# Kernel tuning notes

Hardware: AMD Instinct MI355X
Metric: run time of the kernel (lower is better)

Reference implementation:

```python
import jax, jax.numpy as jnp
import numpy as np

# ---- dims ----
N_NODES = 33      # nodes per graph (33-bus grid)
SEQ     = 24      # time steps per sample
BATCH   = 64      # samples
G       = BATCH * SEQ          # total graphs in the batch
EPG     = 64                   # directed edges per graph
E       = G * EPG              # total edges
N       = G * N_NODES          # total nodes
IN_CH   = 2
HID     = 64
HEADS   = 8
HC      = HID * HEADS          # 512
EDGE_DIM = 3
LSTM1_H = 128
LSTM2_H = 64
N_CLASSES = 4
NEG_SLOPE = 0.2


def setup_inputs() -> dict:
    key = jax.random.key(0)
    ks = jax.random.split(key, 32)
    rng = np.random.default_rng(0)

    # block-structured edge_index: every edge stays inside its own graph
    off = np.repeat(np.arange(G, dtype=np.int64) * N_NODES, EPG)
    src = rng.integers(0, N_NODES, E) + off
    dst = rng.integers(0, N_NODES, E) + off
    edge_index = jnp.asarray(np.stack([src, dst]), dtype=jnp.int32)

    def glorot(k, shape):
        fan = shape[0] + shape[-1]
        s = jnp.sqrt(6.0 / fan).astype(jnp.float32)
        return jax.random.uniform(k, shape, jnp.float32, -s, s)

    inp = dict(
        x=jax.random.normal(ks[0], (N, IN_CH), jnp.float32),
        edge_index=edge_index,
        edge_attr=jax.random.uniform(ks[1], (E, EDGE_DIM), jnp.float32),
        # GATv2 layer 1 (concat=True)
        g1_Wl=glorot(ks[2], (IN_CH, HC)),
        g1_Wr=glorot(ks[3], (IN_CH, HC)),
        g1_We=glorot(ks[4], (EDGE_DIM, HC)),
        g1_att=glorot(ks[5], (HEADS, HID)),
        g1_b=jnp.zeros((HC,), jnp.float32),
        # GATv2 layer 2 (concat=False -> head mean)
        g2_Wl=glorot(ks[6], (HC, HC)),
        g2_Wr=glorot(ks[7], (HC, HC)),
        g2_We=glorot(ks[8], (EDGE_DIM, HC)),
        g2_att=glorot(ks[9], (HEADS, HID)),
        g2_b=jnp.zeros((HID,), jnp.float32),
        # LSTM1: input 33*64=2112 -> 128, gates ordered (i,f,g,o)
        l1_Wih=0.05 * jax.random.normal(ks[10], (4 * LSTM1_H, N_NODES * HID), jnp.float32),
        l1_Whh=0.05 * jax.random.normal(ks[11], (4 * LSTM1_H, LSTM1_H), jnp.float32),
        l1_bih=jnp.zeros((4 * LSTM1_H,), jnp.float32),
        l1_bhh=jnp.zeros((4 * LSTM1_H,), jnp.float32),
        # LSTM2: 128 -> 64
        l2_Wih=0.05 * jax.random.normal(ks[12], (4 * LSTM2_H, LSTM1_H), jnp.float32),
        l2_Whh=0.05 * jax.random.normal(ks[13], (4 * LSTM2_H, LSTM2_H), jnp.float32),
        l2_bih=jnp.zeros((4 * LSTM2_H,), jnp.float32),
        l2_bhh=jnp.zeros((4 * LSTM2_H,), jnp.float32),
        # FC 64 -> n_classes
        fc_W=0.05 * jax.random.normal(ks[14], (N_CLASSES, LSTM2_H), jnp.float32),
        fc_b=jnp.zeros((N_CLASSES,), jnp.float32),
    )
    return inp


def _gatv2(x, edge_attr, src, dst, Wl, Wr, We, att, b, concat):
    """PyG GATv2Conv with edge_dim, add_self_loops semantics omitted is NOT used:
    we follow the message math: m = leaky_relu(xl[src]+xr[dst]+We@e),
    alpha = segment_softmax(<m,att>, dst), out = scatter_add(alpha * xl[src])."""
    n = x.shape[0]
    xl = (x @ Wl).reshape(n, HEADS, HID)      # [N,H,C]
    xr = (x @ Wr).reshape(n, HEADS, HID)
    em = (edge_attr @ We).reshape(-1, HEADS, HID)  # [E,H,C]
    m = jax.nn.leaky_relu(xl[src] + xr[dst] + em, NEG_SLOPE)
    logits = jnp.einsum('ehc,hc->eh', m, att)          # [E,H]
    mx = jax.ops.segment_max(logits, dst, num_segments=n)   # [N,H]
    ex = jnp.exp(logits - mx[dst])
    den = jax.ops.segment_sum(ex, dst, num_segments=n)
    alpha = ex / (den[dst] + 1e-16)                    # [E,H]
    out = jax.ops.segment_sum(xl[src] * alpha[:, :, None], dst, num_segments=n)  # [N,H,C]
    out = out.reshape(n, HC) if concat else out.mean(axis=1)
    return out + b


def _lstm(x, Wih, Whh, bih, bhh, hsz):
    B = x.shape[0]
    h0 = jnp.zeros((B, hsz), x.dtype)
    c0 = jnp.zeros((B, hsz), x.dtype)

    def step(carry, xt):
        h, c = carry
        gates = xt @ Wih.T + h @ Whh.T + bih + bhh
        i, f, g, o = jnp.split(gates, 4, axis=-1)
        i = jax.nn.sigmoid(i); f = jax.nn.sigmoid(f)
        g = jnp.tanh(g);       o = jax.nn.sigmoid(o)
        c = f * c + i * g
        h = o * jnp.tanh(c)
        return (h, c), h

    _, ys = jax.lax.scan(step, (h0, c0), x.transpose(1, 0, 2))  # [T,B,H]
    return ys.transpose(1, 0, 2)


def reference(x, edge_index, edge_attr,
              g1_Wl, g1_Wr, g1_We, g1_att, g1_b,
              g2_Wl, g2_Wr, g2_We, g2_att, g2_b,
              l1_Wih, l1_Whh, l1_bih, l1_bhh,
              l2_Wih, l2_Whh, l2_bih, l2_bhh,
              fc_W, fc_b):
    src, dst = edge_index[0], edge_index[1]
    h = jax.nn.elu(_gatv2(x, edge_attr, src, dst, g1_Wl, g1_Wr, g1_We, g1_att, g1_b, True))
    h = jax.nn.elu(_gatv2(h, edge_attr, src, dst, g2_Wl, g2_Wr, g2_We, g2_att, g2_b, False))
    seq = h.reshape(BATCH, SEQ, N_NODES * HID)          # [B,T,2112]
    seq = _lstm(seq, l1_Wih, l1_Whh, l1_bih, l1_bhh, LSTM1_H)
    seq = _lstm(seq, l2_Wih, l2_Whh, l2_bih, l2_bhh, LSTM2_H)
    last = seq[:, -1, :]                                 # [B,64]
    return last @ fc_W.T + fc_b                          # [B,n_classes]
```

## Files before the change

kernel.cpp:

```cpp
#include <hip/hip_runtime.h>
#include <math.h>

#define N_NODES 33
#define SEQ 24
#define BATCH 64
#define G_GRAPHS (BATCH * SEQ)
#define EPG 64
#define E_EDGES (G_GRAPHS * EPG)
#define N_TOTAL (G_GRAPHS * N_NODES)
#define HID 64
#define HEADS 8
#define HC (HID * HEADS)
#define LSTM1_H 128
#define LSTM2_H 64
#define NEG_SLOPE 0.2f
#define CONV_BLOCKS (128 + 264)

__device__ __forceinline__ float sigmoidf_(float x) { return 1.f / (1.f + expf(-x)); }
__device__ __forceinline__ float eluf_(float x) { return x > 0.f ? x : expm1f(x); }
__device__ __forceinline__ float lreluf_(float x) { return x > 0.f ? x : NEG_SLOPE * x; }

typedef __attribute__((ext_vector_type(4))) float f32x4;
typedef _Float16 half_t;
typedef __attribute__((ext_vector_type(8))) _Float16 halfx8;

__device__ __forceinline__ void gl2lds16(const void* g, void* l) {
  __builtin_amdgcn_global_load_lds(
      (__attribute__((address_space(1))) const unsigned int*)g,
      (__attribute__((address_space(3))) unsigned int*)l, 16, 0, 0);
}

__global__ __launch_bounds__(512) void gat1_kernel(
    const float* __restrict__ x, const int* __restrict__ src, const int* __restrict__ dst,
    const float* __restrict__ ea, const float* __restrict__ Wl, const float* __restrict__ Wr,
    const float* __restrict__ We, const float* __restrict__ att, const float* __restrict__ bias,
    half_t* __restrict__ h1, int g0, int gat_blocks,
    const float* __restrict__ g2Wl, const float* __restrict__ g2Wr,
    half_t* __restrict__ B2, const float* __restrict__ W1, half_t* __restrict__ W1f) {
  const int tid = threadIdx.x;

  __shared__ alignas(16) float Wl_s[2 * 512];
  __shared__ alignas(16) float Wr_s[2 * 512];
  __shared__ alignas(16) float We_s[3 * 512];
  __shared__ alignas(16) float att_s[512];
  __shared__ float xs0_s[N_NODES + 1], xs1_s[N_NODES + 1];
  __shared__ float easX[EPG], easY[EPG], easZ[EPG];
  __shared__ float logit_s[HEADS * 65];
  __shared__ int sloc[EPG], dloc[EPG], deg[N_NODES], start[N_NODES], fill[N_NODES], elist[EPG];
  __shared__ float tr[64 * 65];

  if ((int)blockIdx.x >= gat_blocks) {
    int cb = blockIdx.x - gat_blocks;
    if (cb < 128) {
      int kt = cb & 7, nt = cb >> 3;
      int k0 = kt * 64, n0 = nt * 64;
      int r = tid >> 6, c = tid & 63;
      #pragma unroll
      for (int rr = 0; rr < 8; ++rr) {
        int kl = rr * 8 + r;
        int n = n0 + c;
        float v = (n < 512) ? g2Wl[(size_t)(k0 + kl) * 512 + n]
                            : g2Wr[(size_t)(k0 + kl) * 512 + n - 512];
        tr[kl * 65 + c] = v;
      }
      __syncthreads();
      #pragma unroll
      for (int rr = 0; rr < 8; ++rr) {
        int nl = rr * 8 + r;
        B2[(size_t)(n0 + nl) * 512 + k0 + c] = (half_t)tr[c * 65 + nl];
      }
    } else {
      int base = (cb - 128) * 4096 + tid;
      #pragma unroll
      for (int i = 0; i < 8; ++i) {
        int idx = base + i * 512;
        if (idx < 512 * 2112) W1f[idx] = (half_t)W1[idx];
      }
    }
    return;
  }

  const int g = g0 + blockIdx.x;
  const int nb = g * N_NODES, eb = g * EPG;
  const int lb = blockIdx.x * N_NODES;

  for (int i = tid; i < 1024; i += 512) { Wl_s[i] = Wl[i]; Wr_s[i] = Wr[i]; }
  for (int i = tid; i < 1536; i += 512) We_s[i] = We[i];
  if (tid < 512) att_s[tid] = att[tid];
  if (tid < 2 * N_NODES) {
    float v = x[nb * 2 + tid];
    if (tid & 1) xs1_s[tid >> 1] = v; else xs0_s[tid >> 1] = v;
  }
  if (tid < EPG) {
    easX[tid] = ea[(eb + tid) * 3 + 0];
    easY[tid] = ea[(eb + tid) * 3 + 1];
    easZ[tid] = ea[(eb + tid) * 3 + 2];
    sloc[tid] = src[eb + tid] - nb;
    dloc[tid] = dst[eb + tid] - nb;
  }
  if (tid < N_NODES) { deg[tid] = 0; fill[tid] = 0; }
  __syncthreads();
  if (tid < EPG) atomicAdd(&deg[dloc[tid]], 1);
  __syncthreads();
  if (tid == 0) { int a = 0; for (int n = 0; n < N_NODES; ++n) { start[n] = a; a += deg[n]; } }
  __syncthreads();
  if (tid < EPG) { int d = dloc[tid]; int p = atomicAdd(&fill[d], 1); elist[start[d] + p] = tid; }

  {
    int h = tid >> 6, e = tid & 63;
    int s = sloc[e], d = dloc[e];
    float xs0 = xs0_s[s], xs1 = xs1_s[s], xd0 = xs0_s[d], xd1 = xs1_s[d];
    float e0 = easX[e], e1 = easY[e], e2 = easZ[e];
    float acc = 0.f;
    int base = h * 64;
    #pragma unroll
    for (int c4 = 0; c4 < 16; ++c4) {
      int j = base + c4 * 4;
      f32x4 wl0 = *(const f32x4*)(Wl_s + j);
      f32x4 wl1 = *(const f32x4*)(Wl_s + 512 + j);
      f32x4 wr0 = *(const f32x4*)(Wr_s + j);
      f32x4 wr1 = *(const f32x4*)(Wr_s + 512 + j);
      f32x4 we0 = *(const f32x4*)(We_s + j);
      f32x4 we1 = *(const f32x4*)(We_s + 512 + j);
      f32x4 we2 = *(const f32x4*)(We_s + 1024 + j);
      f32x4 at  = *(const f32x4*)(att_s + j);
      #pragma unroll
      for (int q = 0; q < 4; ++q) {
        float v = xs0 * wl0[q] + xs1 * wl1[q]
                + xd0 * wr0[q] + xd1 * wr1[q]
                + e0 * we0[q] + e1 * we1[q] + e2 * we2[q];
        acc += lreluf_(v) * at[q];
      }
    }
    logit_s[h * 65 + e] = acc;
  }
  __syncthreads();

  {
    int h = tid >> 6, n = tid & 63;
    if (n < N_NODES) {
      int s0 = start[n], dn = deg[n];
      float mx = -1e30f;
      for (int i = 0; i < dn; ++i) mx = fmaxf(mx, logit_s[h * 65 + elist[s0 + i]]);
      float den = 0.f;
      for (int i = 0; i < dn; ++i) den += expf(logit_s[h * 65 + elist[s0 + i]] - mx);
      float inv = 1.f / (den + 1e-16f);
      for (int i = 0; i < dn; ++i) {
        int e = elist[s0 + i];
        logit_s[h * 65 + e] = expf(logit_s[h * 65 + e] - mx) * inv;
      }
    }
  }
  __syncthreads();

  for (int t = tid; t < N_NODES * 64; t += 512) {
    int n = t >> 6, jb = t & 63;
    int j0 = jb * 8, h = jb >> 3;
    f32x4 wa0 = *(const f32x4*)(Wl_s + j0);
    f32x4 wa1 = *(const f32x4*)(Wl_s + j0 + 4);
    f32x4 wb0 = *(const f32x4*)(Wl_s + 512 + j0);
    f32x4 wb1 = *(const f32x4*)(Wl_s + 512 + j0 + 4);
    float acc[8] = {};
    int s0 = start[n], dn = deg[n];
    for (int i = 0; i < dn; ++i) {
      int e = elist[s0 + i]; int s = sloc[e];
      float a = logit_s[h * 65 + e];
      float ax0 = a * xs0_s[s], ax1 = a * xs1_s[s];
      #pragma unroll
      for (int q = 0; q < 4; ++q) {
        acc[q]     += ax0 * wa0[q] + ax1 * wb0[q];
        acc[4 + q] += ax0 * wa1[q] + ax1 * wb1[q];
      }
    }
    f32x4 b0 = *(const f32x4*)(bias + j0);
    f32x4 b1 = *(const f32x4*)(bias + j0 + 4);
    halfx8 vh;
    #pragma unroll
    for (int cc = 0; cc < 8; ++cc) {
      float bb = (cc < 4) ? b0[cc] : b1[cc - 4];
      vh[cc] = (half_t)eluf_(acc[cc] + bb);
    }
    *(halfx8*)(h1 + (size_t)(lb + n) * HC + j0) = vh;
  }
}

template <int WM, int WN, int NP, int K, int SA, int SB, typename TC>
__global__ __launch_bounds__(256) void gemm_f16(
    const half_t* __restrict__ A, const half_t* __restrict__ B,
    TC* __restrict__ C, const float* __restrict__ bias1, const float* __restrict__ bias2,
    int M, int N) {
  constexpr int BM = 32 * WM, BN = 32 * WN;
  constexpr bool BOUNCE = (sizeof(TC) == 2) && (BM == 128) && (BN == 128);
  constexpr int STAGE_HALFS = (BM + BN) * 32 * NP;
  constexpr int CT_HALFS = BOUNCE ? 128 * 132 : 0;
  constexpr int LDS_HALFS = STAGE_HALFS > CT_HALFS ? STAGE_HALFS : CT_HALFS;
  __shared__ half_t lds[LDS_HALFS];
  half_t* A_s = lds;
  half_t* B_s = A_s + NP * BM * 32;

  const int R = M / BM, NT = N / BN;
  int b = blockIdx.x;
  int xcd = b & 7, q = b >> 3;
  int ct = q % NT, rg = q / NT;
  int r = rg * 8 + xcd;
  if (r >= R) return;

  const int tid = threadIdx.x;
  const int wave = tid >> 6, lane = tid & 63;
  const int wm = wave >> 1, wn = wave & 1;
  const int bm = r * BM, bn = ct * BN;

  const int rA = lane >> 2;
  const int swz = (rA & 3) ^ ((rA >> 2) & 3);
  const int cA = ((lane & 3) ^ swz) * 8;

  f32x4 acc[WM][WN];
  #pragma unroll
  for (int tm = 0; tm < WM; ++tm)
    #pragma unroll
    for (int tn = 0; tn < WN; ++tn) acc[tm][tn] = {0.f, 0.f, 0.f, 0.f};

  for (int k0 = 0; k0 < K; k0 += 32 * NP) {
    #pragma unroll
    for (int p = 0; p < NP; ++p) {
      int kk = k0 + p * 32;
      #pragma unroll
      for (int i = 0; i < BM / 64; ++i) {
        int row = i * 64 + wave * 16;
        gl2lds16(A + (size_t)(bm + row + rA) * SA + kk + cA,
                 A_s + p * BM * 32 + row * 32);
      }
      #pragma unroll
      for (int i = 0; i < BN / 64; ++i) {
        int row = i * 64 + wave * 16;
        gl2lds16(B + (size_t)(bn + row + rA) * SB + kk + cA,
                 B_s + p * BN * 32 + row * 32);
      }
    }
    __syncthreads();

    const int fr = lane & 15;
    const int fs = (fr & 3) ^ ((fr >> 2) & 3);
    const int fk = ((lane >> 4) ^ fs) * 8;
    #pragma unroll
    for (int p = 0; p < NP; ++p) {
      const int pA = p * BM * 32, pB = p * BN * 32;
      halfx8 af[WM], bf[WN];
      #pragma unroll
      for (int tm = 0; tm < WM; ++tm) {
        int rr = (wm * WM + tm) * 16 + fr;
        af[tm] = *(const halfx8*)(A_s + pA + rr * 32 + fk);
      }
      #pragma unroll
      for (int tn = 0; tn < WN; ++tn) {
        int rr = (wn * WN + tn) * 16 + fr;
        bf[tn] = *(const halfx8*)(B_s + pB + rr * 32 + fk);
      }
      #pragma unroll
      for (int tm = 0; tm < WM; ++tm)
        #pragma unroll
        for (int tn = 0; tn < WN; ++tn)
          acc[tm][tn] = __builtin_amdgcn_mfma_f32_16x16x32_f16(af[tm], bf[tn], acc[tm][tn], 0, 0, 0);
    }
    __syncthreads();
  }

  const int col0 = lane & 15, rq = (lane >> 4) * 4;
  if constexpr (BOUNCE) {
    half_t* Cs = lds;
    #pragma unroll
    for (int tm = 0; tm < WM; ++tm)
      #pragma unroll
      for (int tn = 0; tn < WN; ++tn) {
        int cl = (wn * WN + tn) * 16 + col0;
        #pragma unroll
        for (int rr = 0; rr < 4; ++rr) {
          int rl = (wm * WM + tm) * 16 + rq + rr;
          Cs[rl * 132 + cl] = (half_t)acc[tm][tn][rr];
        }
      }
    __syncthreads();
    #pragma unroll
    for (int pass = 0; pass < 8; ++pass) {
      int row = pass * 16 + (tid >> 4);
      int col = (tid & 15) * 8;
      halfx8 v = *(const halfx8*)(Cs + row * 132 + col);
      *(halfx8*)((half_t*)C + (size_t)(bm + row) * N + bn + col) = v;
    }
  } else {
    #pragma unroll
    for (int tm = 0; tm < WM; ++tm)
      #pragma unroll
      for (int tn = 0; tn < WN; ++tn) {
        int col = bn + (wn * WN + tn) * 16 + col0;
        float badd = 0.f;
        if (bias1) badd += bias1[col];
        if (bias2) badd += bias2[col];
        #pragma unroll
        for (int rr = 0; rr < 4; ++rr) {
          int row = bm + (wm * WM + tm) * 16 + rq + rr;
          C[(size_t)row * N + col] = (TC)(acc[tm][tn][rr] + badd);
        }
      }
  }
}

__global__ __launch_bounds__(256) void gemm_f16_splitk(
    const half_t* __restrict__ A, const half_t* __restrict__ B,
    float* __restrict__ Cp, const float* __restrict__ bias1, const float* __restrict__ bias2,
    int M, int N) {
  constexpr int SA = 2112;
  __shared__ half_t lds[(64 + 64) * 64];
  half_t* A_s = lds;
  half_t* B_s = A_s + 2 * 64 * 32;

  const int part = blockIdx.y;
  const int koff = part ? 576 + (part - 1) * 512 : 0;
  const int kend = part ? 512 : 576;
  const half_t* Ap = A + koff;
  const half_t* Bp = B + koff;
  float* C = Cp + (size_t)part * M * N;

  const int R = M / 64, NT = N / 64;
  int b = blockIdx.x;
  int xcd = b & 7, q = b >> 3;
  int ct = q % NT, rg = q / NT;
  int r = rg * 8 + xcd;
  if (r >= R) return;

  const int tid = threadIdx.x;
  const int wave = tid >> 6, lane = tid & 63;
  const int wm = wave >> 1, wn = wave & 1;
  const int bm = r * 64, bn = ct * 64;

  const int rA = lane >> 2;
  const int swz = (rA & 3) ^ ((rA >> 2) & 3);
  const int cA = ((lane & 3) ^ swz) * 8;

  f32x4 acc[2][2];
  #pragma unroll
  for (int tm = 0; tm < 2; ++tm)
    #pragma unroll
    for (int tn = 0; tn < 2; ++tn) acc[tm][tn] = {0.f, 0.f, 0.f, 0.f};

  for (int k0 = 0; k0 < kend; k0 += 64) {
    #pragma unroll
    for (int p = 0; p < 2; ++p) {
      int kk = k0 + p * 32;
      int row = wave * 16;
      gl2lds16(Ap + (size_t)(bm + row + rA) * SA + kk + cA,
               A_s + p * 64 * 32 + row * 32);
      gl2lds16(Bp + (size_t)(bn + row + rA) * SA + kk + cA,
               B_s + p * 64 * 32 + row * 32);
    }
    __syncthreads();
    const int fr = lane & 15;
    const int fs = (fr & 3) ^ ((fr >> 2) & 3);
    const int fk = ((lane >> 4) ^ fs) * 8;
    #pragma unroll
    for (int p = 0; p < 2; ++p) {
      const int pA = p * 64 * 32, pB = p * 64 * 32;
      halfx8 af[2], bf[2];
      #pragma unroll
      for (int tm = 0; tm < 2; ++tm) {
        int rr = (wm * 2 + tm) * 16 + fr;
        af[tm] = *(const halfx8*)(A_s + pA + rr * 32 + fk);
      }
      #pragma unroll
      for (int tn = 0; tn < 2; ++tn) {
        int rr = (wn * 2 + tn) * 16 + fr;
        bf[tn] = *(const halfx8*)(B_s + pB + rr * 32 + fk);
      }
      #pragma unroll
      for (int tm = 0; tm < 2; ++tm)
        #pragma unroll
        for (int tn = 0; tn < 2; ++tn)
          acc[tm][tn] = __builtin_amdgcn_mfma_f32_16x16x32_f16(af[tm], bf[tn], acc[tm][tn], 0, 0, 0);
    }
    __syncthreads();
  }

  const int col0 = lane & 15, rq = (lane >> 4) * 4;
  #pragma unroll
  for (int tm = 0; tm < 2; ++tm)
    #pragma unroll
    for (int tn = 0; tn < 2; ++tn) {
      int col = bn + (wn * 2 + tn) * 16 + col0;
      float badd = (part == 0) ? (bias1[col] + bias2[col]) : 0.f;
      #pragma unroll
      for (int rr = 0; rr < 4; ++rr) {
        int row = bm + (wm * 2 + tm) * 16 + rq + rr;
        C[(size_t)row * N + col] = acc[tm][tn][rr] + badd;
      }
    }
}

__global__ __launch_bounds__(512) void gat2_kernel(
    const half_t* __restrict__ xlr, const int* __restrict__ src, const int* __restrict__ dst,
    const float* __restrict__ ea, const float* __restrict__ We,
    const float* __restrict__ att, const float* __restrict__ bias,
    half_t* __restrict__ h2, int g0) {
  __shared__ alignas(16) float We_s[3 * 512];
  __shared__ alignas(16) float att_s[512];
  __shared__ float b_s[HID];
  __shared__ float easX[EPG], easY[EPG], easZ[EPG];
  __shared__ float logit_s[HEADS * 65];
  __shared__ int sloc[EPG], dloc[EPG], deg[N_NODES], start[N_NODES], fill[N_NODES], elist[EPG];

  const int g = g0 + blockIdx.x, tid = threadIdx.x;
  const int nb = g * N_NODES, eb = g * EPG;
  const int lb = blockIdx.x * N_NODES;
  const int wave = tid >> 6, lane = tid & 63;

  for (int i = tid; i < 1536; i += 512) We_s[i] = We[i];
  if (tid < 512) att_s[tid] = att[tid];
  if (tid < HID) b_s[tid] = bias[tid];
  if (tid < EPG) {
    easX[tid] = ea[(eb + tid) * 3 + 0];
    easY[tid] = ea[(eb + tid) * 3 + 1];
    easZ[tid] = ea[(eb + tid) * 3 + 2];
    sloc[tid] = src[eb + tid] - nb;
    dloc[tid] = dst[eb + tid] - nb;
  }
  if (tid < N_NODES) { deg[tid] = 0; fill[tid] = 0; }
  __syncthreads();
  if (tid < EPG) atomicAdd(&deg[dloc[tid]], 1);
  __syncthreads();
  if (tid == 0) { int a = 0; for (int n = 0; n < N_NODES; ++n) { start[n] = a; a += deg[n]; } }
  __syncthreads();
  if (tid < EPG) { int d = dloc[tid]; int p = atomicAdd(&fill[d], 1); elist[start[d] + p] = tid; }
  __syncthreads();

  const int j0 = lane * 8;
  float w0[8], w1[8], w2[8], at8[8];
  #pragma unroll
  for (int q = 0; q < 8; ++q) {
    w0[q] = We_s[j0 + q];
    w1[q] = We_s[512 + j0 + q];
    w2[q] = We_s[1024 + j0 + q];
    at8[q] = att_s[j0 + q];
  }

  for (int e = wave; e < EPG; e += 8) {
    int s = sloc[e], d = dloc[e];
    halfx8 xlv = *((const halfx8*)(xlr + (size_t)(lb + s) * 1024) + lane);
    halfx8 xrv = *((const halfx8*)(xlr + (size_t)(lb + d) * 1024 + 512) + lane);
    float e0 = easX[e], e1 = easY[e], e2 = easZ[e];
    float acc = 0.f;
    #pragma unroll
    for (int q = 0; q < 8; ++q) {
      float v = (float)xlv[q] + (float)xrv[q] + e0 * w0[q] + e1 * w1[q] + e2 * w2[q];
      acc += lreluf_(v) * at8[q];
    }
    acc += __shfl_xor(acc, 1, 64);
    acc += __shfl_xor(acc, 2, 64);
    acc += __shfl_xor(acc, 4, 64);
    if ((lane & 7) == 0) logit_s[(lane >> 3) * 65 + e] = acc;
  }
  __syncthreads();

  {
    int h = tid >> 6, n = tid & 63;
    if (n < N_NODES) {
      int s0 = start[n], dn = deg[n];
      float mx = -1e30f;
      for (int i = 0; i < dn; ++i) mx = fmaxf(mx, logit_s[h * 65 + elist[s0 + i]]);
      float den = 0.f;
      for (int i = 0; i < dn; ++i) den += expf(logit_s[h * 65 + elist[s0 + i]] - mx);
      float inv = 1.f / (den + 1e-16f);
      for (int i = 0; i < dn; ++i) {
        int e = elist[s0 + i];
        logit_s[h * 65 + e] = expf(logit_s[h * 65 + e] - mx) * inv;
      }
    }
  }
  __syncthreads();

  for (int n = wave; n < N_NODES; n += 8) {
    float acc = 0.f;
    int s0 = start[n], dn = deg[n];
    for (int i = 0; i < dn; ++i) {
      int e = elist[s0 + i], s = sloc[e];
      const half_t* row = xlr + (size_t)(lb + s) * 1024 + lane;
      #pragma unroll
      for (int h = 0; h < 8; ++h)
        acc += logit_s[h * 65 + e] * (float)row[h * 64];
    }
    float v = eluf_(acc * 0.125f + b_s[lane]);
    h2[(size_t)(nb + n) * HID + lane] = (half_t)v;
  }
}

__global__ __launch_bounds__(1024, 4) void lstm_all(
    const float* __restrict__ X0, const float* __restrict__ X1,
    const float* __restrict__ X2p, const float* __restrict__ X3,
    const float* __restrict__ Whh1,
    const float* __restrict__ Wih2, const float* __restrict__ bih2,
    const float* __restrict__ bhh2, const float* __restrict__ Whh2,
    const float* __restrict__ fcW, const float* __restrict__ fcb,
    float* __restrict__ out) {
  __shared__ float hs1[LSTM1_H], cs1[LSTM1_H], p1[512], gs1[512];
  __shared__ float Y1s[SEQ][LSTM1_H];
  __shared__ float hs2[LSTM2_H], cs2[LSTM2_H], p2[4 * 256], gs2[256];
  const int tid = threadIdx.x, b = blockIdx.x;
  const int j = tid & 511, half = tid >> 9;

  float4 w1[16];
  {
    const float4* wp = (const float4*)(Whh1 + (size_t)j * LSTM1_H + half * 64);
    #pragma unroll
    for (int q = 0; q < 16; ++q) w1[q] = wp[q];
  }
  if (tid < LSTM1_H) { hs1[tid] = 0.f; cs1[tid] = 0.f; }
  __syncthreads();
  for (int t = 0; t < SEQ; ++t) {
    const float* hb = hs1 + half * 64;
    float acc = 0.f;
    #pragma unroll
    for (int q = 0; q < 16; ++q) {
      acc += w1[q].x * hb[4 * q] + w1[q].y * hb[4 * q + 1]
           + w1[q].z * hb[4 * q + 2] + w1[q].w * hb[4 * q + 3];
    }
    if (half) p1[j] = acc;
    __syncthreads();
    if (!half) {
      size_t xo = ((size_t)b * SEQ + t) * 512 + j;
      gs1[j] = acc + p1[j] + X0[xo] + X1[xo] + X2p[xo] + X3[xo];
    }
    __syncthreads();
    if (tid < LSTM1_H) {
      float ig = sigmoidf_(gs1[tid]);
      float fg = sigmoidf_(gs1[LSTM1_H + tid]);
      float gg = tanhf(gs1[2 * LSTM1_H + tid]);
      float og = sigmoidf_(gs1[3 * LSTM1_H + tid]);
      float c = fg * cs1[tid] + ig * gg;
      cs1[tid] = c;
      float h = og * tanhf(c);
      hs1[tid] = h;
      Y1s[t][tid] = h;
    }
    __syncthreads();
  }

  const int j2 = tid & 255, qt = tid >> 8;
  float4 w2x[8], w2h[4];
  {
    const float4* wxp = (const float4*)(Wih2 + (size_t)j2 * LSTM1_H + qt * 32);
    #pragma unroll
    for (int q = 0; q < 8; ++q) w2x[q] = wxp[q];
    const float4* whp = (const float4*)(Whh2 + (size_t)j2 * LSTM2_H + qt * 16);
    #pragma unroll
    for (int q = 0; q < 4; ++q) w2h[q] = whp[q];
  }
  if (tid < LSTM2_H) { hs2[tid] = 0.f; cs2[tid] = 0.f; }
  __syncthreads();
  for (int t = 0; t < SEQ; ++t) {
    const float* y = Y1s[t] + qt * 32;
    const float* hb = hs2 + qt * 16;
    float acc = 0.f;
    #pragma unroll
    for (int q = 0; q < 8; ++q) {
      acc += w2x[q].x * y[4 * q] + w2x[q].y * y[4 * q + 1]
           + w2x[q].z * y[4 * q + 2] + w2x[q].w * y[4 * q + 3];
    }
    #pragma unroll
    for (int q = 0; q < 4; ++q) {
      acc += w2h[q].x * hb[4 * q] + w2h[q].y * hb[4 * q + 1]
           + w2h[q].z * hb[4 * q + 2] + w2h[q].w * hb[4 * q + 3];
    }
    p2[qt * 256 + j2] = acc;
    __syncthreads();
    if (qt == 0)
      gs2[j2] = p2[j2] + p2[256 + j2] + p2[512 + j2] + p2[768 + j2]
              + bih2[j2] + bhh2[j2];
    __syncthreads();
    if (tid < LSTM2_H) {
      float ig = sigmoidf_(gs2[tid]);
      float fg = sigmoidf_(gs2[LSTM2_H + tid]);
      float gg = tanhf(gs2[2 * LSTM2_H + tid]);
      float og = sigmoidf_(gs2[3 * LSTM2_H + tid]);
      float c = fg * cs2[tid] + ig * gg;
      cs2[tid] = c;
      hs2[tid] = og * tanhf(c);
    }
    __syncthreads();
  }
  if (tid < 4) {
    float acc = fcb[tid];
    #pragma unroll
    for (int k = 0; k < LSTM2_H; ++k) acc += fcW[tid * LSTM2_H + k] * hs2[k];
    out[b * 4 + tid] = acc;
  }
}

extern "C" void kernel_launch(void* const* d_in, const int* in_sizes, int n_in,
                              void* d_out, int out_size, void* d_ws, size_t ws_size,
                              hipStream_t stream) {
  const float* x       = (const float*)d_in[0];
  const int*   eidx    = (const int*)d_in[1];
  const float* eattr   = (const float*)d_in[2];
  const float* g1_Wl   = (const float*)d_in[3];
  const float* g1_Wr   = (const float*)d_in[4];
  const float* g1_We   = (const float*)d_in[5];
  const float* g1_att  = (const float*)d_in[6];
  const float* g1_b    = (const float*)d_in[7];
  const float* g2_Wl   = (const float*)d_in[8];
  const float* g2_Wr   = (const float*)d_in[9];
  const float* g2_We   = (const float*)d_in[10];
  const float* g2_att  = (const float*)d_in[11];
  const float* g2_b    = (const float*)d_in[12];
  const float* l1_Wih  = (const float*)d_in[13];
  const float* l1_Whh  = (const float*)d_in[14];
  const float* l1_bih  = (const float*)d_in[15];
  const float* l1_bhh  = (const float*)d_in[16];
  const float* l2_Wih  = (const float*)d_in[17];
  const float* l2_Whh  = (const float*)d_in[18];
  const float* l2_bih  = (const float*)d_in[19];
  const float* l2_bhh  = (const float*)d_in[20];
  const float* fc_W    = (const float*)d_in[21];
  const float* fc_b    = (const float*)d_in[22];
  float* out = (float*)d_out;

  const int* src = eidx;
  const int* dst = eidx + E_EDGES;

  const int cand[5] = {1, 2, 3, 4, 6};
  int nchunks = 0;
  half_t *h1 = nullptr, *xlr2c = nullptr, *h2 = nullptr, *B2 = nullptr, *W1f = nullptr;
  float *X1p = nullptr;
  int chunk_g = 0, chunk_n = 0;
  for (int ci = 0; ci < 5; ++ci) {
    int C = cand[ci];
    int CG = G_GRAPHS / C, CN = CG * N_NODES;
    char* p = (char*)d_ws;
    auto alloc = [&](size_t bytes) { char* r = p; p += (bytes + 255) & ~(size_t)255; return r; };
    half_t* t_h1    = (half_t*)alloc((size_t)CN * HC * 2);
    half_t* t_xlr2c = (half_t*)alloc((size_t)CN * 1024 * 2);
    half_t* t_h2    = (half_t*)alloc((size_t)G_GRAPHS * 2112 * 2);
    half_t* t_B2    = (half_t*)alloc((size_t)1024 * 512 * 2);
    half_t* t_W1f   = (half_t*)alloc((size_t)512 * 2112 * 2);
    float*  t_X1p   = (float*)alloc((size_t)4 * G_GRAPHS * 512 * 4);
    if ((size_t)(p - (char*)d_ws) <= ws_size) {
      nchunks = C; chunk_g = CG; chunk_n = CN;
      h1 = t_h1; xlr2c = t_xlr2c; h2 = t_h2; B2 = t_B2; W1f = t_W1f;
      X1p = t_X1p;
      break;
    }
  }
  if (nchunks == 0) return;

  for (int c = 0; c < nchunks; ++c) {
    int g0 = c * chunk_g;
    int extra = (c == 0) ? CONV_BLOCKS : 0;
    gat1_kernel<<<chunk_g + extra, 512, 0, stream>>>(
        x, src, dst, eattr, g1_Wl, g1_Wr, g1_We, g1_att, g1_b, h1, g0, chunk_g,
        g2_Wl, g2_Wr, B2, l1_Wih, W1f);
    int R = chunk_n / 128, NT = 1024 / 128;
    int gblocks = 8 * ((R + 7) / 8) * NT;
    gemm_f16<4, 4, 2, HC, HC, HC, half_t><<<gblocks, 256, 0, stream>>>(
        h1, B2, xlr2c, (const float*)nullptr, (const float*)nullptr,
        chunk_n, 1024);
    gat2_kernel<<<chunk_g, 512, 0, stream>>>(xlr2c, src, dst, eattr, g2_We,
                                             g2_att, g2_b, h2, g0);
  }

  {
    dim3 grid(192, 4);
    gemm_f16_splitk<<<grid, 256, 0, stream>>>(h2, W1f, X1p, l1_bih, l1_bhh,
                                              G_GRAPHS, 512);
  }

  {
    size_t PS = (size_t)G_GRAPHS * 512;
    lstm_all<<<BATCH, 1024, 0, stream>>>(X1p, X1p + PS, X1p + 2 * PS, X1p + 3 * PS,
                                         l1_Whh, l2_Wih, l2_bih, l2_bhh, l2_Whh,
                                         fc_W, fc_b, out);
  }
}
```

Measured before the change: 349.1 us.

## Replace layer-2 projection GEMM with 256x256 tile, 4-stage pipelined kernel

Swaps the templated 128x128 GEMM that computes the layer-2 left/right projections for a dedicated 256x256-tile kernel. It uses 512 threads, a 4-slot LDS ring with 3 tiles of prefetch gated by explicit vmcnt waits, and raised wave priority around the MFMA block. The larger tile halves global re-reads of A and B per output, and the deeper pipeline overlaps loads with compute. The cost is a full 128 KB of LDS and 128 accumulator registers per lane, which limits occupancy. The chunk candidate 4 is dropped so that chunk node counts stay divisible by 256.

New measurement: 359.5 us. 1.03x slower.

```diff
diff --git a/kernel.cpp b/kernel.cpp
--- a/kernel.cpp
+++ b/kernel.cpp
@@ -184,124 +184,106 @@
   }
 }
 
-template <int WM, int WN, int NP, int K, int SA, int SB, typename TC>
-__global__ __launch_bounds__(256) void gemm_f16(
+__global__ __launch_bounds__(512, 2) void gemm256(
     const half_t* __restrict__ A, const half_t* __restrict__ B,
-    TC* __restrict__ C, const float* __restrict__ bias1, const float* __restrict__ bias2,
-    int M, int N) {
-  constexpr int BM = 32 * WM, BN = 32 * WN;
-  constexpr bool BOUNCE = (sizeof(TC) == 2) && (BM == 128) && (BN == 128);
-  constexpr int STAGE_HALFS = (BM + BN) * 32 * NP;
-  constexpr int CT_HALFS = BOUNCE ? 128 * 132 : 0;
-  constexpr int LDS_HALFS = STAGE_HALFS > CT_HALFS ? STAGE_HALFS : CT_HALFS;
-  __shared__ half_t lds[LDS_HALFS];
-  half_t* A_s = lds;
-  half_t* B_s = A_s + NP * BM * 32;
-
-  const int R = M / BM, NT = N / BN;
+    half_t* __restrict__ C, int M) {
+  __shared__ alignas(16) half_t lds[65536];
+
+  const int R = M >> 8;
   int b = blockIdx.x;
   int xcd = b & 7, q = b >> 3;
-  int ct = q % NT, rg = q / NT;
+  int ct = q & 3, rg = q >> 2;
   int r = rg * 8 + xcd;
   if (r >= R) return;
 
   const int tid = threadIdx.x;
   const int wave = tid >> 6, lane = tid & 63;
-  const int wm = wave >> 1, wn = wave & 1;
-  const int bm = r * BM, bn = ct * BN;
+  const int wm = wave >> 2, wn = wave & 3;
+  const int bm = r << 8, bn = ct << 8;
 
   const int rA = lane >> 2;
-  const int swz = (rA & 3) ^ ((rA >> 2) & 3);
-  const int cA = ((lane & 3) ^ swz) * 8;
-
-  f32x4 acc[WM][WN];
+  const int swzS = (rA & 3) ^ ((rA >> 2) & 3);
+  const int cA = ((lane & 3) ^ swzS) * 8;
+
+  const int fr = lane & 15;
+  const int fs = (fr & 3) ^ ((fr >> 2) & 3);
+  const int fk = ((lane >> 4) ^ fs) * 8;
+
+  f32x4 acc[8][4];
   #pragma unroll
-  for (int tm = 0; tm < WM; ++tm)
-    #pragma unroll
-    for (int tn = 0; tn < WN; ++tn) acc[tm][tn] = {0.f, 0.f, 0.f, 0.f};
-
-  for (int k0 = 0; k0 < K; k0 += 32 * NP) {
-    #pragma unroll
-    for (int p = 0; p < NP; ++p) {
-      int kk = k0 + p * 32;
-      #pragma unroll
-      for (int i = 0; i < BM / 64; ++i) {
-        int row = i * 64 + wave * 16;
-        gl2lds16(A + (size_t)(bm + row + rA) * SA + kk + cA,
-                 A_s + p * BM * 32 + row * 32);
-      }
-      #pragma unroll
-      for (int i = 0; i < BN / 64; ++i) {
-        int row = i * 64 + wave * 16;
-        gl2lds16(B + (size_t)(bn + row + rA) * SB + kk + cA,
-                 B_s + p * BN * 32 + row * 32);
-      }
-    }
-    __syncthreads();
-
-    const int fr = lane & 15;
-    const int fs = (fr & 3) ^ ((fr >> 2) & 3);
-    const int fk = ((lane >> 4) ^ fs) * 8;
-    #pragma unroll
-    for (int p = 0; p < NP; ++p) {
-      const int pA = p * BM * 32, pB = p * BN * 32;
-      halfx8 af[WM], bf[WN];
-      #pragma unroll
-      for (int tm = 0; tm < WM; ++tm) {
-        int rr = (wm * WM + tm) * 16 + fr;
-        af[tm] = *(const halfx8*)(A_s + pA + rr * 32 + fk);
-      }
-      #pragma unroll
-      for (int tn = 0; tn < WN; ++tn) {
-        int rr = (wn * WN + tn) * 16 + fr;
-        bf[tn] = *(const halfx8*)(B_s + pB + rr * 32 + fk);
-      }
-      #pragma unroll
-      for (int tm = 0; tm < WM; ++tm)
+  for (int tm = 0; tm < 8; ++tm)
+    #pragma unroll
+    for (int tn = 0; tn < 4; ++tn) acc[tm][tn] = {0.f, 0.f, 0.f, 0.f};
+
+  auto stage = [&](int kt, int slot) {
+    half_t* As = lds + slot * 16384;
+    half_t* Bs = As + 8192;
+    const int koff = kt * 32 + cA;
+    #pragma unroll
+    for (int i = 0; i < 2; ++i) {
+      int row = i * 128 + wave * 16;
+      gl2lds16(A + (size_t)(bm + row + rA) * 512 + koff, As + row * 32);
+      gl2lds16(B + (size_t)(bn + row + rA) * 512 + koff, Bs + row * 32);
+    }
+  };
+
+  stage(0, 0);
+  stage(1, 1);
+  stage(2, 2);
+
+  for (int kt = 0; kt < 16; ++kt) {
+    if (kt < 14)       asm volatile("s_waitcnt vmcnt(8)" ::: "memory");
+    else if (kt == 14) asm volatile("s_waitcnt vmcnt(4)" ::: "memory");
+    else               asm volatile("s_waitcnt vmcnt(0)" ::: "memory");
+    __builtin_amdgcn_s_barrier();
+    asm volatile("" ::: "memory");
+
+    if (kt + 3 < 16) stage(kt + 3, (kt + 3) & 3);
+
+    const half_t* As = lds + (kt & 3) * 16384;
+    const half_t* Bs = As + 8192;
+
+    halfx8 bf[4];
+    #pragma unroll
+    for (int tn = 0; tn < 4; ++tn)
+      bf[tn] = *(const halfx8*)(Bs + (wn * 64 + tn * 16 + fr) * 32 + fk);
+
+    __builtin_amdgcn_s_setprio(1);
+    #pragma unroll
+    for (int tm = 0; tm < 8; ++tm) {
+      halfx8 af = *(const halfx8*)(As + (wm * 128 + tm * 16 + fr) * 32 + fk);
+      #pragma unroll
+      for (int tn = 0; tn < 4; ++tn)
+        acc[tm][tn] = __builtin_amdgcn_mfma_f32_16x16x32_f16(af, bf[tn], acc[tm][tn], 0, 0, 0);
+    }
+    __builtin_amdgcn_s_setprio(0);
+  }
+
+  half_t* Cs = lds;
+  const int rq = (lane >> 4) * 4;
+  const int cl0 = lane & 15;
+  #pragma unroll 1
+  for (int mh = 0; mh < 2; ++mh) {
+    __syncthreads();
+    if (wm == mh) {
+      #pragma unroll
+      for (int tm = 0; tm < 8; ++tm)
         #pragma unroll
-        for (int tn = 0; tn < WN; ++tn)
-          acc[tm][tn] = __builtin_amdgcn_mfma_f32_16x16x32_f16(af[tm], bf[tn], acc[tm][tn], 0, 0, 0);
-    }
-    __syncthreads();
-  }
-
-  const int col0 = lane & 15, rq = (lane >> 4) * 4;
-  if constexpr (BOUNCE) {
-    half_t* Cs = lds;
-    #pragma unroll
-    for (int tm = 0; tm < WM; ++tm)
-      #pragma unroll
-      for (int tn = 0; tn < WN; ++tn) {
-        int cl = (wn * WN + tn) * 16 + col0;
-        #pragma unroll
-        for (int rr = 0; rr < 4; ++rr) {
-          int rl = (wm * WM + tm) * 16 + rq + rr;
-          Cs[rl * 132 + cl] = (half_t)acc[tm][tn][rr];
+        for (int tn = 0; tn < 4; ++tn) {
+          int cl = wn * 64 + tn * 16 + cl0;
+          #pragma unroll
+          for (int rr = 0; rr < 4; ++rr)
+            Cs[(tm * 16 + rq + rr) * 264 + cl] = (half_t)acc[tm][tn][rr];
         }
-      }
-    __syncthreads();
-    #pragma unroll
-    for (int pass = 0; pass < 8; ++pass) {
-      int row = pass * 16 + (tid >> 4);
-      int col = (tid & 15) * 8;
-      halfx8 v = *(const halfx8*)(Cs + row * 132 + col);
-      *(halfx8*)((half_t*)C + (size_t)(bm + row) * N + bn + col) = v;
-    }
-  } else {
-    #pragma unroll
-    for (int tm = 0; tm < WM; ++tm)
-      #pragma unroll
-      for (int tn = 0; tn < WN; ++tn) {
-        int col = bn + (wn * WN + tn) * 16 + col0;
-        float badd = 0.f;
-        if (bias1) badd += bias1[col];
-        if (bias2) badd += bias2[col];
-        #pragma unroll
-        for (int rr = 0; rr < 4; ++rr) {
-          int row = bm + (wm * WM + tm) * 16 + rq + rr;
-          C[(size_t)row * N + col] = (TC)(acc[tm][tn][rr] + badd);
-        }
-      }
+    }
+    __syncthreads();
+    #pragma unroll
+    for (int i = 0; i < 8; ++i) {
+      int rr2 = i * 16 + (tid >> 5);
+      int cc = (tid & 31) * 8;
+      halfx8 v = *(const halfx8*)(Cs + rr2 * 264 + cc);
+      *(halfx8*)(C + (size_t)(bm + mh * 128 + rr2) * 1024 + bn + cc) = v;
+    }
   }
 }
 
@@ -624,12 +606,12 @@
   const int* src = eidx;
   const int* dst = eidx + E_EDGES;
 
-  const int cand[5] = {1, 2, 3, 4, 6};
+  const int cand[4] = {1, 2, 3, 6};
   int nchunks = 0;
   half_t *h1 = nullptr, *xlr2c = nullptr, *h2 = nullptr, *B2 = nullptr, *W1f = nullptr;
   float *X1p = nullptr;
   int chunk_g = 0, chunk_n = 0;
-  for (int ci = 0; ci < 5; ++ci) {
+  for (int ci = 0; ci < 4; ++ci) {
     int C = cand[ci];
     int CG = G_GRAPHS / C, CN = CG * N_NODES;
     char* p = (char*)d_ws;
@@ -655,11 +637,9 @@
     gat1_kernel<<<chunk_g + extra, 512, 0, stream>>>(
         x, src, dst, eattr, g1_Wl, g1_Wr, g1_We, g1_att, g1_b, h1, g0, chunk_g,
         g2_Wl, g2_Wr, B2, l1_Wih, W1f);
-    int R = chunk_n / 128, NT = 1024 / 128;
-    int gblocks = 8 * ((R + 7) / 8) * NT;
-    gemm_f16<4, 4, 2, HC, HC, HC, half_t><<<gblocks, 256, 0, stream>>>(
-        h1, B2, xlr2c, (const float*)nullptr, (const float*)nullptr,
-        chunk_n, 1024);
+    int R = chunk_n / 256;
+    int gblocks = 8 * ((R + 7) / 8) * 4;
+    gemm256<<<gblocks, 512, 0, stream>>>(h1, B2, xlr2c, chunk_n);
     gat2_kernel<<<chunk_g, 512, 0, stream>>>(xlr2c, src, dst, eattr, g2_We,
                                              g2_att, g2_b, h2, g0);
   }
```
